# Performance work log

Measured on AMD Instinct MI355X. Metric: run time of the kernel, lower is better.

## Reference

```python
import jax, jax.numpy as jnp
import numpy as np

C_IN = 256
C_OUT = 256
NUM_HEADS = 4
C_HEAD = C_OUT // NUM_HEADS  # 64
ALPHA = 0.2
NEG_FILL = -9e15


def setup_inputs() -> dict:
    key = jax.random.key(0)
    k1, k2, k3, k4, k5 = jax.random.split(key, 5)
    B, N = 1, 4096
    node_feats = jax.random.normal(k1, (B, N, C_IN), dtype=jnp.float32)
    adj_matrix = jax.random.randint(k2, (B, N, N), 0, 2, dtype=jnp.int32)
    # xavier_uniform with gain=1.414 on projection weight (fan_in=C_IN, fan_out=C_OUT)
    lim_w = 1.414 * np.sqrt(6.0 / (C_IN + C_OUT))
    W = jax.random.uniform(k3, (C_IN, C_OUT), dtype=jnp.float32, minval=-lim_w, maxval=lim_w)
    b = jnp.zeros((C_OUT,), dtype=jnp.float32)
    lim_a = 1.414 * np.sqrt(6.0 / (NUM_HEADS + 2 * C_HEAD))
    a = jax.random.uniform(k4, (NUM_HEADS, 2 * C_HEAD), dtype=jnp.float32, minval=-lim_a, maxval=lim_a)
    return {"node_feats": node_feats, "adj_matrix": adj_matrix, "W": W, "b": b, "a": a}


def reference(node_feats, adj_matrix, W, b, a):
    B, N, _ = node_feats.shape
    # linear projection -> (B, N, H, C_HEAD)
    feats = (node_feats @ W + b).reshape(B, N, NUM_HEADS, C_HEAD)
    # attention logit for edge (i -> j): a_src . h_i + a_dst . h_j, per head
    a_src, a_dst = a[:, :C_HEAD], a[:, C_HEAD:]
    src = jnp.einsum('bnhc,hc->bnh', feats, a_src)  # indexed by row i
    dst = jnp.einsum('bnhc,hc->bnh', feats, a_dst)  # indexed by col j
    logits = src[:, :, None, :] + dst[:, None, :, :]  # (B, N, N, H)
    logits = jnp.where(logits >= 0, logits, ALPHA * logits)  # LeakyReLU(0.2)
    attn = jnp.where(adj_matrix[..., None] == 1, logits, NEG_FILL)
    probs = jax.nn.softmax(attn, axis=2)  # softmax over source nodes j
    out = jnp.einsum('bijh,bjhc->bihc', probs, feats)
    return out.reshape(B, N, NUM_HEADS * C_HEAD)  # concat heads
```

## Files before the change

kernel.cpp:

```cpp
#include <hip/hip_runtime.h>

#define NN 4096
#define C 256
#define NH 4
#define CH 64
#define JSPLIT 8
#define JSLICE (NN / JSPLIT)
#define NJT (JSLICE / 32)

typedef float f32x4 __attribute__((ext_vector_type(4)));
typedef __bf16 b16x8 __attribute__((ext_vector_type(8)));
typedef unsigned short u16x8 __attribute__((ext_vector_type(8)));
typedef unsigned int u32x4 __attribute__((ext_vector_type(4)));

__device__ inline float fast_exp2(float x) {
#if __has_builtin(__builtin_amdgcn_exp2f)
  return __builtin_amdgcn_exp2f(x);
#else
  return exp2f(x);
#endif
}

__device__ inline unsigned pack2bf(float f0, float f1) {
  unsigned u0 = __float_as_uint(f0) + 0x8000u;
  unsigned u1 = __float_as_uint(f1) + 0x8000u;
  return __builtin_amdgcn_perm(u1, u0, 0x07060302u);
}

__global__ __launch_bounds__(256) void k_prep(
    const int* __restrict__ adj, const float* __restrict__ X,
    const float* __restrict__ W, unsigned char* __restrict__ packed,
    unsigned short* __restrict__ Xbf, unsigned short* __restrict__ WT) {
  const int b = blockIdx.x, t = threadIdx.x;
  if (b < 8192) {
    const int idx = b * 256 + t;
    const int4 a0 = *(const int4*)(adj + (size_t)idx * 8);
    const int4 a1 = *(const int4*)(adj + (size_t)idx * 8 + 4);
    unsigned m = 0;
    m |= (a0.x != 0) ? 1u : 0u;   m |= (a0.y != 0) ? 2u : 0u;
    m |= (a0.z != 0) ? 4u : 0u;   m |= (a0.w != 0) ? 8u : 0u;
    m |= (a1.x != 0) ? 16u : 0u;  m |= (a1.y != 0) ? 32u : 0u;
    m |= (a1.z != 0) ? 64u : 0u;  m |= (a1.w != 0) ? 128u : 0u;
    packed[idx] = (unsigned char)m;
  } else if (b < 9216) {
    const int idx = (b - 8192) * 256 + t;
    const float4 v = ((const float4*)X)[idx];
    uint2 st;
    st.x = pack2bf(v.x, v.y);
    st.y = pack2bf(v.z, v.w);
    ((uint2*)Xbf)[idx] = st;
  } else {
    const int c = b - 9216;
    const float w = W[(size_t)t * C + c];
    WT[(size_t)c * C + t] = (unsigned short)((__float_as_uint(w) + 0x8000u) >> 16);
  }
}

__global__ __launch_bounds__(256) void k_feats(
    const unsigned short* __restrict__ Xbf, const unsigned short* __restrict__ WT,
    const float* __restrict__ bias, const float* __restrict__ av,
    unsigned short* __restrict__ F, float* __restrict__ srcv,
    float2* __restrict__ dstT2) {
  const int i0 = blockIdx.x * 16;
  const int h = threadIdx.x >> 6;
  const int lane = threadIdx.x & 63;
  const int q = lane >> 4, n = lane & 15;
  const int c0 = h * CH;
  const float LOG2E = 1.4426950408889634f;

  const f32x4 zero = {0.f, 0.f, 0.f, 0.f};
  f32x4 acc[4];
#pragma unroll
  for (int g = 0; g < 4; ++g) acc[g] = zero;

  const unsigned short* ap = Xbf + (size_t)(i0 + n) * C + q * 8;
#pragma unroll
  for (int kt = 0; kt < 8; ++kt) {
    const b16x8 aF = __builtin_bit_cast(b16x8, *(const u16x8*)(ap + kt * 32));
#pragma unroll
    for (int g = 0; g < 4; ++g) {
      const b16x8 bF = __builtin_bit_cast(b16x8,
          *(const u16x8*)(WT + (size_t)(c0 + g * 16 + n) * C + kt * 32 + q * 8));
      acc[g] = __builtin_amdgcn_mfma_f32_16x16x32_bf16(aF, bF, acc[g], 0, 0, 0);
    }
  }

  float fb[4][4], asv[4], adv[4];
#pragma unroll
  for (int g = 0; g < 4; ++g) {
    const float bs = bias[c0 + g * 16 + n];
    asv[g] = av[h * 128 + g * 16 + n];
    adv[g] = av[h * 128 + 64 + g * 16 + n];
#pragma unroll
    for (int r = 0; r < 4; ++r) fb[g][r] = acc[g][r] + bs;
  }
  const int jt = i0 >> 5, half = (i0 >> 4) & 1;
  const int qp = half * 2 + (q >> 1);
#pragma unroll
  for (int g = 0; g < 4; ++g) {
    uint2 st;
    st.x = pack2bf(fb[g][0], fb[g][1]);
    st.y = pack2bf(fb[g][2], fb[g][3]);
    *(uint2*)(F + ((size_t)((jt * NH + h) * 4 + g)) * 512 + (qp * 16 + n) * 8 + 4 * (q & 1)) = st;
  }
#pragma unroll
  for (int r = 0; r < 4; ++r) {
    float p = 0.f, d = 0.f;
#pragma unroll
    for (int g = 0; g < 4; ++g) {
      p = fmaf(fb[g][r], asv[g], p);
      d = fmaf(fb[g][r], adv[g], d);
    }
#pragma unroll
    for (int m = 1; m < 16; m <<= 1) {
      p += __shfl_xor(p, m);
      d += __shfl_xor(d, m);
    }
    if (n == 0) {
      const int row = i0 + q * 4 + r;
      srcv[(size_t)row * NH + h] = p;
      const float dL = d * LOG2E;
      dstT2[(size_t)h * NN + row] = make_float2(dL, 0.2f * dL);
    }
  }
}

__global__ __launch_bounds__(256, 4) void k_attn(
    const unsigned char* __restrict__ packed,
    const unsigned short* __restrict__ F,
    const float* __restrict__ srcv, const float2* __restrict__ dstT2,
    _Float16* __restrict__ pacc, float* __restrict__ lpart) {
  const int slice = blockIdx.x;
  const int i0 = blockIdx.y * 32;
  const int h = threadIdx.x >> 6;
  const int lane = threadIdx.x & 63;
  const int q = lane >> 4, n = lane & 15;
  const int jbase = slice * JSLICE;

  const float LOG2E = 1.4426950408889634f;
  const int r0 = i0 + n, r1 = i0 + 16 + n;
  const float s0 = srcv[(size_t)r0 * NH + h];
  const float s1 = srcv[(size_t)r1 * NH + h];
  const float xm0 = s0 + 16.0f, xm1 = s1 + 16.0f;
  const float m20 = fmaxf(xm0, 0.2f * xm0) * LOG2E;
  const float m21 = fmaxf(xm1, 0.2f * xm1) * LOG2E;
  const float u0 = fmaf(s0, LOG2E, -m20), w0 = fmaf(0.2f * s0, LOG2E, -m20);
  const float u1 = fmaf(s1, LOG2E, -m21), w1 = fmaf(0.2f * s1, LOG2E, -m21);

  const f32x4 zero = {0.f, 0.f, 0.f, 0.f};
  f32x4 acc0[4], acc1[4], lacc0 = zero, lacc1 = zero;
#pragma unroll
  for (int g = 0; g < 4; ++g) { acc0[g] = zero; acc1[g] = zero; }

  u16x8 ou;
#pragma unroll
  for (int jj = 0; jj < 8; ++jj) ou[jj] = 0x3F80;
  const b16x8 ones = __builtin_bit_cast(b16x8, ou);

  const u32x4 m40 = *(const u32x4*)(packed + (size_t)r0 * 512 + (jbase >> 3) + q * 16);
  const u32x4 m41 = *(const u32x4*)(packed + (size_t)r1 * 512 + (jbase >> 3) + q * 16);

  const float* dp2 = (const float*)(dstT2 + (size_t)h * NN + jbase);
  const unsigned short* fp = F + ((size_t)((jbase >> 5) * NH + h) * 4) * 512 + lane * 8;

#pragma unroll
  for (int a = 0; a < 4; ++a) {
#pragma unroll
    for (int b = 0; b < 4; ++b) {
      const int jt = a * 4 + b;
      b16x8 bF[4];
#pragma unroll
      for (int g = 0; g < 4; ++g)
        bF[g] = __builtin_bit_cast(b16x8,
            *(const u16x8*)(fp + (size_t)(jt * NH * 4 + g) * 512));

      const unsigned Mb0 = (unsigned(__shfl((int)m40[b], a * 16 + n)) >> (q * 8)) & 0xffu;
      const unsigned Mb1 = (unsigned(__shfl((int)m41[b], a * 16 + n)) >> (q * 8)) & 0xffu;

      const float* dq = dp2 + jt * 64 + q * 16;
      const float4 dd0 = *(const float4*)(dq);
      const float4 dd1 = *(const float4*)(dq + 4);
      const float4 dd2 = *(const float4*)(dq + 8);
      const float4 dd3 = *(const float4*)(dq + 12);
      const float4 dd[4] = {dd0, dd1, dd2, dd3};

      u32x4 pk0, pk1;
#pragma unroll
      for (int k = 0; k < 4; ++k) {
        const float a00 = fmaxf(dd[k].x + u0, dd[k].y + w0);
        const float a01 = fmaxf(dd[k].z + u0, dd[k].w + w0);
        const float a10 = fmaxf(dd[k].x + u1, dd[k].y + w1);
        const float a11 = fmaxf(dd[k].z + u1, dd[k].w + w1);
        const float e00 = fast_exp2((Mb0 & (1u << (2 * k))) ? a00 : -200.0f);
        const float e01 = fast_exp2((Mb0 & (2u << (2 * k))) ? a01 : -200.0f);
        const float e10 = fast_exp2((Mb1 & (1u << (2 * k))) ? a10 : -200.0f);
        const float e11 = fast_exp2((Mb1 & (2u << (2 * k))) ? a11 : -200.0f);
        pk0[k] = pack2bf(e00, e01);
        pk1[k] = pack2bf(e10, e11);
      }
      const b16x8 E0 = __builtin_bit_cast(b16x8, pk0);
      const b16x8 E1 = __builtin_bit_cast(b16x8, pk1);
#pragma unroll
      for (int g = 0; g < 4; ++g) {
        acc0[g] = __builtin_amdgcn_mfma_f32_16x16x32_bf16(E0, bF[g], acc0[g], 0, 0, 0);
        acc1[g] = __builtin_amdgcn_mfma_f32_16x16x32_bf16(E1, bF[g], acc1[g], 0, 0, 0);
      }
      lacc0 = __builtin_amdgcn_mfma_f32_16x16x32_bf16(E0, ones, lacc0, 0, 0, 0);
      lacc1 = __builtin_amdgcn_mfma_f32_16x16x32_bf16(E1, ones, lacc1, 0, 0, 0);
    }
  }

#pragma unroll
  for (int g = 0; g < 4; ++g)
#pragma unroll
    for (int r = 0; r < 4; ++r) {
      const int col = h * CH + g * 16 + n;
      pacc[((size_t)slice * NN + i0 + q * 4 + r) * C + col] = (_Float16)acc0[g][r];
      pacc[((size_t)slice * NN + i0 + 16 + q * 4 + r) * C + col] = (_Float16)acc1[g][r];
    }
  if (n == 0) {
#pragma unroll
    for (int r = 0; r < 4; ++r) {
      lpart[((size_t)slice * NN + i0 + q * 4 + r) * NH + h] = lacc0[r];
      lpart[((size_t)slice * NN + i0 + 16 + q * 4 + r) * NH + h] = lacc1[r];
    }
  }
}

__global__ __launch_bounds__(256) void k_final(
    const _Float16* __restrict__ pacc, const float* __restrict__ lpart,
    float* __restrict__ out) {
  const int i = blockIdx.x;
  const int c = threadIdx.x;
  const int h = c >> 6;
  float l = 0.f, sa = 0.f;
#pragma unroll
  for (int sp = 0; sp < JSPLIT; ++sp) {
    l += lpart[((size_t)sp * NN + i) * NH + h];
    sa += (float)pacc[((size_t)sp * NN + i) * C + c];
  }
  out[(size_t)i * C + c] = sa / l;
}

extern "C" void kernel_launch(void* const* d_in, const int* in_sizes, int n_in,
                              void* d_out, int out_size, void* d_ws, size_t ws_size,
                              hipStream_t stream) {
  const float* nf   = (const float*)d_in[0];
  const int* adj    = (const int*)d_in[1];
  const float* W    = (const float*)d_in[2];
  const float* bias = (const float*)d_in[3];
  const float* av   = (const float*)d_in[4];
  float* out = (float*)d_out;

  char* ws = (char*)d_ws;
  unsigned char* packed  = (unsigned char*)ws;
  unsigned short* Xbf    = (unsigned short*)(ws + (2u << 20));
  unsigned short* WT     = (unsigned short*)(ws + (4u << 20));
  unsigned short* F      = (unsigned short*)(ws + (4u << 20) + (256u << 10));
  float* srcv   = (float*)(ws + (6u << 20) + (256u << 10));
  float2* dstT2 = (float2*)(ws + (6u << 20) + (320u << 10));
  float* lpart  = (float*)(ws + (6u << 20) + (448u << 10));
  _Float16* pacc = (_Float16*)(ws + (8u << 20));

  k_prep<<<9472, 256, 0, stream>>>(adj, nf, W, packed, Xbf, WT);
  k_feats<<<NN / 16, 256, 0, stream>>>(Xbf, WT, bias, av, F, srcv, dstT2);
  dim3 g2(JSPLIT, NN / 32);
  k_attn<<<g2, 256, 0, stream>>>(packed, F, srcv, dstT2, pacc, lpart);
  k_final<<<NN, 256, 0, stream>>>(pacc, lpart, out);
}
```

Baseline: 139.9 us.

## Halve attention row tile to 16 and double j-slice per block

The attention kernel now handles 16 query rows per block instead of 32 and splits the source dimension into 4 slices instead of 8. Each block therefore covers twice as many j tiles. This halves the partial-accumulator traffic written to and read back by the final reduction. In exchange, each loaded F tile and dst vector now feeds only one row group instead of two, so global loads per MFMA double. The longer serial loop per block also reduces the within-block parallelism available to hide latency.

Measured after the change: 173.5 us. +24.1%, slower.

```diff
diff --git a/kernel.cpp b/kernel.cpp
--- a/kernel.cpp
+++ b/kernel.cpp
@@ -4,7 +4,7 @@
 #define C 256
 #define NH 4
 #define CH 64
-#define JSPLIT 8
+#define JSPLIT 4
 #define JSLICE (NN / JSPLIT)
 #define NJT (JSLICE / 32)
 
@@ -131,40 +131,37 @@
     const float* __restrict__ srcv, const float2* __restrict__ dstT2,
     _Float16* __restrict__ pacc, float* __restrict__ lpart) {
   const int slice = blockIdx.x;
-  const int i0 = blockIdx.y * 32;
+  const int i0 = blockIdx.y * 16;
   const int h = threadIdx.x >> 6;
   const int lane = threadIdx.x & 63;
   const int q = lane >> 4, n = lane & 15;
   const int jbase = slice * JSLICE;
+  const int row = i0 + n;
 
   const float LOG2E = 1.4426950408889634f;
-  const int r0 = i0 + n, r1 = i0 + 16 + n;
-  const float s0 = srcv[(size_t)r0 * NH + h];
-  const float s1 = srcv[(size_t)r1 * NH + h];
-  const float xm0 = s0 + 16.0f, xm1 = s1 + 16.0f;
+  const float s0 = srcv[(size_t)row * NH + h];
+  const float xm0 = s0 + 16.0f;
   const float m20 = fmaxf(xm0, 0.2f * xm0) * LOG2E;
-  const float m21 = fmaxf(xm1, 0.2f * xm1) * LOG2E;
   const float u0 = fmaf(s0, LOG2E, -m20), w0 = fmaf(0.2f * s0, LOG2E, -m20);
-  const float u1 = fmaf(s1, LOG2E, -m21), w1 = fmaf(0.2f * s1, LOG2E, -m21);
 
   const f32x4 zero = {0.f, 0.f, 0.f, 0.f};
-  f32x4 acc0[4], acc1[4], lacc0 = zero, lacc1 = zero;
-#pragma unroll
-  for (int g = 0; g < 4; ++g) { acc0[g] = zero; acc1[g] = zero; }
+  f32x4 acc[4], lacc = zero;
+#pragma unroll
+  for (int g = 0; g < 4; ++g) acc[g] = zero;
 
   u16x8 ou;
 #pragma unroll
   for (int jj = 0; jj < 8; ++jj) ou[jj] = 0x3F80;
   const b16x8 ones = __builtin_bit_cast(b16x8, ou);
 
-  const u32x4 m40 = *(const u32x4*)(packed + (size_t)r0 * 512 + (jbase >> 3) + q * 16);
-  const u32x4 m41 = *(const u32x4*)(packed + (size_t)r1 * 512 + (jbase >> 3) + q * 16);
+  const u32x4 m4a = *(const u32x4*)(packed + (size_t)row * 512 + (jbase >> 3) + q * 16);
+  const u32x4 m4b = *(const u32x4*)(packed + (size_t)row * 512 + (jbase >> 3) + 64 + q * 16);
 
   const float* dp2 = (const float*)(dstT2 + (size_t)h * NN + jbase);
   const unsigned short* fp = F + ((size_t)((jbase >> 5) * NH + h) * 4) * 512 + lane * 8;
 
 #pragma unroll
-  for (int a = 0; a < 4; ++a) {
+  for (int a = 0; a < 8; ++a) {
 #pragma unroll
     for (int b = 0; b < 4; ++b) {
       const int jt = a * 4 + b;
@@ -174,8 +171,8 @@
         bF[g] = __builtin_bit_cast(b16x8,
             *(const u16x8*)(fp + (size_t)(jt * NH * 4 + g) * 512));
 
-      const unsigned Mb0 = (unsigned(__shfl((int)m40[b], a * 16 + n)) >> (q * 8)) & 0xffu;
-      const unsigned Mb1 = (unsigned(__shfl((int)m41[b], a * 16 + n)) >> (q * 8)) & 0xffu;
+      const int mword = (a < 4) ? (int)m4a[b] : (int)m4b[b];
+      const unsigned Mb = (unsigned(__shfl(mword, (a & 3) * 16 + n)) >> (q * 8)) & 0xffu;
 
       const float* dq = dp2 + jt * 64 + q * 16;
       const float4 dd0 = *(const float4*)(dq);
@@ -184,29 +181,20 @@
       const float4 dd3 = *(const float4*)(dq + 12);
       const float4 dd[4] = {dd0, dd1, dd2, dd3};
 
-      u32x4 pk0, pk1;
+      u32x4 pk;
 #pragma unroll
       for (int k = 0; k < 4; ++k) {
-        const float a00 = fmaxf(dd[k].x + u0, dd[k].y + w0);
-        const float a01 = fmaxf(dd[k].z + u0, dd[k].w + w0);
-        const float a10 = fmaxf(dd[k].x + u1, dd[k].y + w1);
-        const float a11 = fmaxf(dd[k].z + u1, dd[k].w + w1);
-        const float e00 = fast_exp2((Mb0 & (1u << (2 * k))) ? a00 : -200.0f);
-        const float e01 = fast_exp2((Mb0 & (2u << (2 * k))) ? a01 : -200.0f);
-        const float e10 = fast_exp2((Mb1 & (1u << (2 * k))) ? a10 : -200.0f);
-        const float e11 = fast_exp2((Mb1 & (2u << (2 * k))) ? a11 : -200.0f);
-        pk0[k] = pack2bf(e00, e01);
-        pk1[k] = pack2bf(e10, e11);
+        const float a0 = fmaxf(dd[k].x + u0, dd[k].y + w0);
+        const float a1 = fmaxf(dd[k].z + u0, dd[k].w + w0);
+        const float e0 = fast_exp2((Mb & (1u << (2 * k))) ? a0 : -200.0f);
+        const float e1 = fast_exp2((Mb & (2u << (2 * k))) ? a1 : -200.0f);
+        pk[k] = pack2bf(e0, e1);
       }
-      const b16x8 E0 = __builtin_bit_cast(b16x8, pk0);
-      const b16x8 E1 = __builtin_bit_cast(b16x8, pk1);
-#pragma unroll
-      for (int g = 0; g < 4; ++g) {
-        acc0[g] = __builtin_amdgcn_mfma_f32_16x16x32_bf16(E0, bF[g], acc0[g], 0, 0, 0);
-        acc1[g] = __builtin_amdgcn_mfma_f32_16x16x32_bf16(E1, bF[g], acc1[g], 0, 0, 0);
-      }
-      lacc0 = __builtin_amdgcn_mfma_f32_16x16x32_bf16(E0, ones, lacc0, 0, 0, 0);
-      lacc1 = __builtin_amdgcn_mfma_f32_16x16x32_bf16(E1, ones, lacc1, 0, 0, 0);
+      const b16x8 E = __builtin_bit_cast(b16x8, pk);
+#pragma unroll
+      for (int g = 0; g < 4; ++g)
+        acc[g] = __builtin_amdgcn_mfma_f32_16x16x32_bf16(E, bF[g], acc[g], 0, 0, 0);
+      lacc = __builtin_amdgcn_mfma_f32_16x16x32_bf16(E, ones, lacc, 0, 0, 0);
     }
   }
 
@@ -215,15 +203,12 @@
 #pragma unroll
     for (int r = 0; r < 4; ++r) {
       const int col = h * CH + g * 16 + n;
-      pacc[((size_t)slice * NN + i0 + q * 4 + r) * C + col] = (_Float16)acc0[g][r];
-      pacc[((size_t)slice * NN + i0 + 16 + q * 4 + r) * C + col] = (_Float16)acc1[g][r];
+      pacc[((size_t)slice * NN + i0 + q * 4 + r) * C + col] = (_Float16)acc[g][r];
     }
   if (n == 0) {
 #pragma unroll
-    for (int r = 0; r < 4; ++r) {
-      lpart[((size_t)slice * NN + i0 + q * 4 + r) * NH + h] = lacc0[r];
-      lpart[((size_t)slice * NN + i0 + 16 + q * 4 + r) * NH + h] = lacc1[r];
-    }
+    for (int r = 0; r < 4; ++r)
+      lpart[((size_t)slice * NN + i0 + q * 4 + r) * NH + h] = lacc[r];
   }
 }
 
@@ -264,7 +249,7 @@
 
   k_prep<<<9472, 256, 0, stream>>>(adj, nf, W, packed, Xbf, WT);
   k_feats<<<NN / 16, 256, 0, stream>>>(Xbf, WT, bias, av, F, srcv, dstT2);
-  dim3 g2(JSPLIT, NN / 32);
+  dim3 g2(JSPLIT, NN / 16);
   k_attn<<<g2, 256, 0, stream>>>(packed, F, srcv, dstT2, pacc, lpart);
   k_final<<<NN, 256, 0, stream>>>(pacc, lpart, out);
 }
```

## Pre-permute packed adjacency mask so attention kernel avoids cross-lane shuffles

Applied to the files above, without the earlier changes.

The prep kernel now writes the bit-packed adjacency mask in a slice-major, MFMA-lane-friendly order, so each lane's 16-byte mask load directly holds the bits it needs for every j-tile. This removes the per-tile __shfl operations and shift/mask arithmetic in the attention inner loop, replacing them with register byte extraction. The cost is a strided, less coalesced read of the int32 adjacency matrix in the prep kernel, which may hurt the bandwidth-bound mask packing.

Measured after the change: 141.6 us. About the same (+1.2%).

```diff
diff --git a/kernel.cpp b/kernel.cpp
--- a/kernel.cpp
+++ b/kernel.cpp
@@ -34,8 +34,13 @@
   const int b = blockIdx.x, t = threadIdx.x;
   if (b < 8192) {
     const int idx = b * 256 + t;
-    const int4 a0 = *(const int4*)(adj + (size_t)idx * 8);
-    const int4 a1 = *(const int4*)(adj + (size_t)idx * 8 + 4);
+    const int jt = idx & 15;
+    const int q = (idx >> 4) & 3;
+    const int row = (idx >> 6) & 4095;
+    const int slice = idx >> 18;
+    const int j0 = slice * 512 + jt * 32 + q * 8;
+    const int4 a0 = *(const int4*)(adj + (size_t)row * NN + j0);
+    const int4 a1 = *(const int4*)(adj + (size_t)row * NN + j0 + 4);
     unsigned m = 0;
     m |= (a0.x != 0) ? 1u : 0u;   m |= (a0.y != 0) ? 2u : 0u;
     m |= (a0.z != 0) ? 4u : 0u;   m |= (a0.w != 0) ? 8u : 0u;
@@ -157,57 +162,50 @@
   for (int jj = 0; jj < 8; ++jj) ou[jj] = 0x3F80;
   const b16x8 ones = __builtin_bit_cast(b16x8, ou);
 
-  const u32x4 m40 = *(const u32x4*)(packed + (size_t)r0 * 512 + (jbase >> 3) + q * 16);
-  const u32x4 m41 = *(const u32x4*)(packed + (size_t)r1 * 512 + (jbase >> 3) + q * 16);
+  const u32x4 m40 = *(const u32x4*)(packed + (size_t)slice * 262144 + r0 * 64 + q * 16);
+  const u32x4 m41 = *(const u32x4*)(packed + (size_t)slice * 262144 + r1 * 64 + q * 16);
 
   const float* dp2 = (const float*)(dstT2 + (size_t)h * NN + jbase);
   const unsigned short* fp = F + ((size_t)((jbase >> 5) * NH + h) * 4) * 512 + lane * 8;
 
 #pragma unroll
-  for (int a = 0; a < 4; ++a) {
-#pragma unroll
-    for (int b = 0; b < 4; ++b) {
-      const int jt = a * 4 + b;
-      b16x8 bF[4];
-#pragma unroll
-      for (int g = 0; g < 4; ++g)
-        bF[g] = __builtin_bit_cast(b16x8,
-            *(const u16x8*)(fp + (size_t)(jt * NH * 4 + g) * 512));
-
-      const unsigned Mb0 = (unsigned(__shfl((int)m40[b], a * 16 + n)) >> (q * 8)) & 0xffu;
-      const unsigned Mb1 = (unsigned(__shfl((int)m41[b], a * 16 + n)) >> (q * 8)) & 0xffu;
-
-      const float* dq = dp2 + jt * 64 + q * 16;
-      const float4 dd0 = *(const float4*)(dq);
-      const float4 dd1 = *(const float4*)(dq + 4);
-      const float4 dd2 = *(const float4*)(dq + 8);
-      const float4 dd3 = *(const float4*)(dq + 12);
-      const float4 dd[4] = {dd0, dd1, dd2, dd3};
-
-      u32x4 pk0, pk1;
-#pragma unroll
-      for (int k = 0; k < 4; ++k) {
-        const float a00 = fmaxf(dd[k].x + u0, dd[k].y + w0);
-        const float a01 = fmaxf(dd[k].z + u0, dd[k].w + w0);
-        const float a10 = fmaxf(dd[k].x + u1, dd[k].y + w1);
-        const float a11 = fmaxf(dd[k].z + u1, dd[k].w + w1);
-        const float e00 = fast_exp2((Mb0 & (1u << (2 * k))) ? a00 : -200.0f);
-        const float e01 = fast_exp2((Mb0 & (2u << (2 * k))) ? a01 : -200.0f);
-        const float e10 = fast_exp2((Mb1 & (1u << (2 * k))) ? a10 : -200.0f);
-        const float e11 = fast_exp2((Mb1 & (2u << (2 * k))) ? a11 : -200.0f);
-        pk0[k] = pack2bf(e00, e01);
-        pk1[k] = pack2bf(e10, e11);
-      }
-      const b16x8 E0 = __builtin_bit_cast(b16x8, pk0);
-      const b16x8 E1 = __builtin_bit_cast(b16x8, pk1);
-#pragma unroll
-      for (int g = 0; g < 4; ++g) {
-        acc0[g] = __builtin_amdgcn_mfma_f32_16x16x32_bf16(E0, bF[g], acc0[g], 0, 0, 0);
-        acc1[g] = __builtin_amdgcn_mfma_f32_16x16x32_bf16(E1, bF[g], acc1[g], 0, 0, 0);
-      }
-      lacc0 = __builtin_amdgcn_mfma_f32_16x16x32_bf16(E0, ones, lacc0, 0, 0, 0);
-      lacc1 = __builtin_amdgcn_mfma_f32_16x16x32_bf16(E1, ones, lacc1, 0, 0, 0);
-    }
+  for (int jt = 0; jt < NJT; ++jt) {
+    b16x8 bF[4];
+#pragma unroll
+    for (int g = 0; g < 4; ++g)
+      bF[g] = __builtin_bit_cast(b16x8,
+          *(const u16x8*)(fp + (size_t)(jt * NH * 4 + g) * 512));
+
+    const unsigned Mb0 = (m40[jt >> 2] >> ((jt & 3) * 8)) & 0xffu;
+    const unsigned Mb1 = (m41[jt >> 2] >> ((jt & 3) * 8)) & 0xffu;
+
+    const float* dq = dp2 + jt * 64 + q * 16;
+    const float4 dd[4] = {*(const float4*)(dq), *(const float4*)(dq + 4),
+                          *(const float4*)(dq + 8), *(const float4*)(dq + 12)};
+
+    u32x4 pk0, pk1;
+#pragma unroll
+    for (int k = 0; k < 4; ++k) {
+      const float a00 = fmaxf(dd[k].x + u0, dd[k].y + w0);
+      const float a01 = fmaxf(dd[k].z + u0, dd[k].w + w0);
+      const float a10 = fmaxf(dd[k].x + u1, dd[k].y + w1);
+      const float a11 = fmaxf(dd[k].z + u1, dd[k].w + w1);
+      const float e00 = fast_exp2((Mb0 & (1u << (2 * k))) ? a00 : -200.0f);
+      const float e01 = fast_exp2((Mb0 & (2u << (2 * k))) ? a01 : -200.0f);
+      const float e10 = fast_exp2((Mb1 & (1u << (2 * k))) ? a10 : -200.0f);
+      const float e11 = fast_exp2((Mb1 & (2u << (2 * k))) ? a11 : -200.0f);
+      pk0[k] = pack2bf(e00, e01);
+      pk1[k] = pack2bf(e10, e11);
+    }
+    const b16x8 E0 = __builtin_bit_cast(b16x8, pk0);
+    const b16x8 E1 = __builtin_bit_cast(b16x8, pk1);
+#pragma unroll
+    for (int g = 0; g < 4; ++g) {
+      acc0[g] = __builtin_amdgcn_mfma_f32_16x16x32_bf16(E0, bF[g], acc0[g], 0, 0, 0);
+      acc1[g] = __builtin_amdgcn_mfma_f32_16x16x32_bf16(E1, bF[g], acc1[g], 0, 0, 0);
+    }
+    lacc0 = __builtin_amdgcn_mfma_f32_16x16x32_bf16(E0, ones, lacc0, 0, 0, 0);
+    lacc1 = __builtin_amdgcn_mfma_f32_16x16x32_bf16(E1, ones, lacc1, 0, 0, 0);
   }
 
 #pragma unroll
```
